# Kernel optimization log

Measured on AMD Instinct MI355X. Metric: run time of the kernel, lower is better.

The kernel has to match this reference:

```python
import jax, jax.numpy as jnp
import numpy as np

N_EMBED = 1024
HEAD_SIZE = 64
BLOCK_SIZE = 2048


def setup_inputs() -> dict:
    key = jax.random.key(0)
    kx, kk, kv = jax.random.split(key, 3)
    x = jax.random.normal(kx, (8, 2048, N_EMBED), dtype=jnp.float32)
    # nn.Linear(n_embed, head_size, bias=False): weight [head_size, n_embed]
    scale = 1.0 / np.sqrt(N_EMBED)
    W_k = jax.random.uniform(kk, (HEAD_SIZE, N_EMBED), dtype=jnp.float32, minval=-scale, maxval=scale)
    W_v = jax.random.uniform(kv, (HEAD_SIZE, N_EMBED), dtype=jnp.float32, minval=-scale, maxval=scale)
    return {"x": x, "W_k": W_k, "W_v": W_v}


def reference(x, W_k, W_v):
    # Faithful to source: q = self.key(x) (query projection is unused in the original forward)
    T = x.shape[1]
    k = jnp.einsum('btc,hc->bth', x, W_k)   # [B,T,H]
    q = k                                    # source bug: q uses key projection
    wei = jnp.einsum('bth,bsh->bts', q, k) * (HEAD_SIZE ** -0.5)  # [B,T,T]
    causal = jnp.tril(jnp.ones((T, T), dtype=bool))
    wei = jnp.where(causal, wei, -jnp.inf)
    wei = jax.nn.softmax(wei, axis=-1)
    v = jnp.einsum('btc,hc->bth', x, W_v)
    out = jnp.einsum('bts,bsh->bth', wei, v)
    return out
```

## Files before the change

kernel.cpp:

```cpp
#include <hip/hip_runtime.h>


typedef __bf16 bf16;
typedef __bf16 bf16x4 __attribute__((ext_vector_type(4)));
typedef __bf16 bf16x8 __attribute__((ext_vector_type(8)));
typedef float  floatx4 __attribute__((ext_vector_type(4)));

#define T_LEN 2048
#define HEAD  64
#define CEMB  1024

static __device__ __forceinline__ bf16x8 cvt2(float4 a, float4 b) {
    bf16x8 r;
    r[0] = (bf16)a.x; r[1] = (bf16)a.y; r[2] = (bf16)a.z; r[3] = (bf16)a.w;
    r[4] = (bf16)b.x; r[5] = (bf16)b.y; r[6] = (bf16)b.z; r[7] = (bf16)b.w;
    return r;
}

__global__ __launch_bounds__(256) void wconv_kernel(const float* __restrict__ Wk,
                                                    const float* __restrict__ Wv,
                                                    bf16* __restrict__ Wb) {
    int i = (blockIdx.x * 256 + threadIdx.x) * 4;
    const float* src = (i < 64 * 1024) ? (Wk + i) : (Wv + (i - 64 * 1024));
    float4 f = *(const float4*)src;
    bf16x4 v;
    v[0] = (bf16)f.x; v[1] = (bf16)f.y; v[2] = (bf16)f.z; v[3] = (bf16)f.w;
    *(bf16x4*)&Wb[i] = v;
}

__global__ __launch_bounds__(256) void proj_kernel(const float* __restrict__ x,
                                                   const bf16* __restrict__ Wb,
                                                   bf16* __restrict__ Kbuf,
                                                   bf16* __restrict__ Vt) {
    __shared__ __align__(16) bf16 As[2][32][72];
    __shared__ __align__(16) bf16 Bs[2][128][72];

    const int tid  = threadIdx.x;
    const int wave = tid >> 6;
    const int lane = tid & 63;
    const int quad = lane >> 4;
    const int low  = lane & 15;

    const long row0 = (long)blockIdx.x * 32;

    const int a_row = tid >> 3;
    const int a_col = (tid & 7) * 8;
    const int b_row = tid >> 1;
    const int b_col = (tid & 1) * 32;

    const float* abase = x + (row0 + a_row) * CEMB + a_col;
    const bf16*  bbase = Wb + b_row * CEMB + b_col;

    const int strip = wave & 1;
    const int nq    = (wave >> 1) * 4;

    floatx4 acc[4];
#pragma unroll
    for (int i = 0; i < 4; ++i) acc[i] = (floatx4){0.f, 0.f, 0.f, 0.f};

    float4 apf0 = ((const float4*)abase)[0], apf1 = ((const float4*)abase)[1];
    float4 bpf0 = ((const float4*)bbase)[0], bpf1 = ((const float4*)bbase)[1];
    float4 bpf2 = ((const float4*)bbase)[2], bpf3 = ((const float4*)bbase)[3];
    *(bf16x8*)&As[0][a_row][a_col] = cvt2(apf0, apf1);
    *(float4*)&Bs[0][b_row][b_col]      = bpf0;
    *(float4*)&Bs[0][b_row][b_col + 8]  = bpf1;
    *(float4*)&Bs[0][b_row][b_col + 16] = bpf2;
    *(float4*)&Bs[0][b_row][b_col + 24] = bpf3;
    __syncthreads();

    int buf = 0;
    for (int s = 0; s < 16; ++s) {
        const bool more = (s < 15);
        if (more) {
            const int k0 = (s + 1) * 64;
            apf0 = ((const float4*)(abase + k0))[0]; apf1 = ((const float4*)(abase + k0))[1];
            bpf0 = ((const float4*)(bbase + k0))[0]; bpf1 = ((const float4*)(bbase + k0))[1];
            bpf2 = ((const float4*)(bbase + k0))[2]; bpf3 = ((const float4*)(bbase + k0))[3];
        }
#pragma unroll
        for (int ks = 0; ks < 2; ++ks) {
            bf16x8 afrag = *(const bf16x8*)&As[buf][strip * 16 + low][ks * 32 + quad * 8];
#pragma unroll
            for (int i = 0; i < 4; ++i) {
                bf16x8 bfrag = *(const bf16x8*)&Bs[buf][(nq + i) * 16 + low][ks * 32 + quad * 8];
                acc[i] = __builtin_amdgcn_mfma_f32_16x16x32_bf16(afrag, bfrag, acc[i], 0, 0, 0);
            }
        }
        if (more) {
            const int nb = buf ^ 1;
            *(bf16x8*)&As[nb][a_row][a_col] = cvt2(apf0, apf1);
            *(float4*)&Bs[nb][b_row][b_col]      = bpf0;
            *(float4*)&Bs[nb][b_row][b_col + 8]  = bpf1;
            *(float4*)&Bs[nb][b_row][b_col + 16] = bpf2;
            *(float4*)&Bs[nb][b_row][b_col + 24] = bpf3;
            __syncthreads();
            buf = nb;
        }
    }

    const long bidx  = row0 >> 11;
    const int  tloc0 = (int)(row0 & 2047);
#pragma unroll
    for (int i = 0; i < 4; ++i) {
#pragma unroll
        for (int r = 0; r < 4; ++r) {
            int trow = tloc0 + strip * 16 + quad * 4 + r;
            int cl   = (nq + i) * 16 + low;
            bf16 val = (bf16)acc[i][r];
            if (cl < HEAD) Kbuf[(bidx * T_LEN + trow) * HEAD + cl] = val;
            else           Vt[(bidx * HEAD + (cl - HEAD)) * T_LEN + trow] = val;
        }
    }
}

__global__ __launch_bounds__(256) void attn_kernel(const bf16* __restrict__ Kbuf,
                                                   const bf16* __restrict__ Vt,
                                                   float* __restrict__ Opart,
                                                   float* __restrict__ lpart) {
    __shared__ __align__(16) bf16 Ks[2][64][72];
    __shared__ __align__(16) bf16 Vs[2][64][72];
    __shared__ __align__(16) bf16 Ps[64][72];

    const int tid  = threadIdx.x;
    const int wave = tid >> 6;
    const int lane = tid & 63;
    const int quad = lane >> 4;
    const int low  = lane & 15;

    const int c  = blockIdx.x & 7;
    const int qb = (blockIdx.x >> 3) & 31;
    const int b  = blockIdx.x >> 8;

    const bf16* kbase = Kbuf + (long)b * T_LEN * HEAD;
    const bf16* vbase = Vt + (long)b * HEAD * T_LEN;

    const bf16* qrow = kbase + (qb * 64 + wave * 16 + low) * HEAD + quad * 8;
    const bf16x8 qf0 = *(const bf16x8*)(qrow);
    const bf16x8 qf1 = *(const bf16x8*)(qrow + 32);

    bf16x8 ones;
#pragma unroll
    for (int i = 0; i < 8; ++i) ones[i] = (bf16)1.0f;

    floatx4 o[4], ol;
#pragma unroll
    for (int nt = 0; nt < 4; ++nt) o[nt] = (floatx4){0.f, 0.f, 0.f, 0.f};
    ol = (floatx4){0.f, 0.f, 0.f, 0.f};

    const int s_row = tid >> 2;
    const int s_col = (tid & 3) * 16;
    const bf16* ksrc = kbase + s_row * HEAD + s_col;
    const bf16* vsrc = vbase + (long)s_row * T_LEN + s_col;

    if (c <= qb) {
        float4 kpf0 = *(const float4*)(ksrc + c * 4096);
        float4 kpf1 = *(const float4*)(ksrc + c * 4096 + 8);
        float4 vpf0 = *(const float4*)(vsrc + c * 64);
        float4 vpf1 = *(const float4*)(vsrc + c * 64 + 8);
        *(float4*)&Ks[0][s_row][s_col]     = kpf0;
        *(float4*)&Ks[0][s_row][s_col + 8] = kpf1;
        *(float4*)&Vs[0][s_row][s_col]     = vpf0;
        *(float4*)&Vs[0][s_row][s_col + 8] = vpf1;
        __syncthreads();

        int buf = 0;
        for (int j = c; j <= qb; j += 8) {
            const bool more = (j + 8 <= qb);
            if (more) {
                kpf0 = *(const float4*)(ksrc + (j + 8) * 4096);
                kpf1 = *(const float4*)(ksrc + (j + 8) * 4096 + 8);
                vpf0 = *(const float4*)(vsrc + (j + 8) * 64);
                vpf1 = *(const float4*)(vsrc + (j + 8) * 64 + 8);
            }

            floatx4 s_[4];
#pragma unroll
            for (int nt = 0; nt < 4; ++nt) {
                bf16x8 kf0 = *(const bf16x8*)&Ks[buf][nt * 16 + low][quad * 8];
                bf16x8 kf1 = *(const bf16x8*)&Ks[buf][nt * 16 + low][32 + quad * 8];
                floatx4 z = (floatx4){0.f, 0.f, 0.f, 0.f};
                z = __builtin_amdgcn_mfma_f32_16x16x32_bf16(qf0, kf0, z, 0, 0, 0);
                z = __builtin_amdgcn_mfma_f32_16x16x32_bf16(qf1, kf1, z, 0, 0, 0);
                s_[nt] = z;
            }

            const bool diag = (j == qb);
#pragma unroll
            for (int nt = 0; nt < 4; ++nt) {
#pragma unroll
                for (int r = 0; r < 4; ++r) {
                    float p = __builtin_amdgcn_exp2f(s_[nt][r] * 0.180336880f);
                    if (diag && (nt * 16 + low) > (wave * 16 + quad * 4 + r)) p = 0.f;
                    Ps[wave * 16 + quad * 4 + r][nt * 16 + low] = (bf16)p;
                }
            }

            bf16x8 pf0 = *(const bf16x8*)&Ps[wave * 16 + low][quad * 8];
            bf16x8 pf1 = *(const bf16x8*)&Ps[wave * 16 + low][32 + quad * 8];
#pragma unroll
            for (int nt = 0; nt < 4; ++nt) {
                bf16x8 vf0 = *(const bf16x8*)&Vs[buf][nt * 16 + low][quad * 8];
                bf16x8 vf1 = *(const bf16x8*)&Vs[buf][nt * 16 + low][32 + quad * 8];
                o[nt] = __builtin_amdgcn_mfma_f32_16x16x32_bf16(pf0, vf0, o[nt], 0, 0, 0);
                o[nt] = __builtin_amdgcn_mfma_f32_16x16x32_bf16(pf1, vf1, o[nt], 0, 0, 0);
            }
            ol = __builtin_amdgcn_mfma_f32_16x16x32_bf16(pf0, ones, ol, 0, 0, 0);
            ol = __builtin_amdgcn_mfma_f32_16x16x32_bf16(pf1, ones, ol, 0, 0, 0);

            if (more) {
                const int nb = buf ^ 1;
                *(float4*)&Ks[nb][s_row][s_col]     = kpf0;
                *(float4*)&Ks[nb][s_row][s_col + 8] = kpf1;
                *(float4*)&Vs[nb][s_row][s_col]     = vpf0;
                *(float4*)&Vs[nb][s_row][s_col + 8] = vpf1;
                __syncthreads();
                buf = nb;
            }
        }
    }

    float* ob = Opart + (long)blockIdx.x * 4096;
#pragma unroll
    for (int nt = 0; nt < 4; ++nt) {
#pragma unroll
        for (int r = 0; r < 4; ++r) {
            int row = wave * 16 + quad * 4 + r;
            ob[row * 64 + nt * 16 + low] = o[nt][r];
        }
    }
    if (low == 0) {
#pragma unroll
        for (int r = 0; r < 4; ++r)
            lpart[(long)blockIdx.x * 64 + wave * 16 + quad * 4 + r] = ol[r];
    }
}

__global__ __launch_bounds__(256) void attn_combine(const float* __restrict__ Opart,
                                                    const float* __restrict__ lpart,
                                                    float* __restrict__ out) {
    const int tile = blockIdx.x;
    const int tid  = threadIdx.x;
    const int row  = tid >> 2;
    const int col0 = (tid & 3) * 16;

    const float* ob = Opart + (long)tile * 8 * 4096 + row * 64 + col0;
    const float* lb = lpart + (long)tile * 8 * 64 + row;

    float l = 0.f;
#pragma unroll
    for (int ch = 0; ch < 8; ++ch) l += lb[ch * 64];
    float rl = 1.0f / l;

    float4 s0 = (float4){0.f, 0.f, 0.f, 0.f}, s1 = s0, s2 = s0, s3 = s0;
#pragma unroll
    for (int ch = 0; ch < 8; ++ch) {
        const float4* p = (const float4*)(ob + ch * 4096);
        float4 a = p[0], b = p[1], c = p[2], d = p[3];
        s0.x += a.x; s0.y += a.y; s0.z += a.z; s0.w += a.w;
        s1.x += b.x; s1.y += b.y; s1.z += b.z; s1.w += b.w;
        s2.x += c.x; s2.y += c.y; s2.z += c.z; s2.w += c.w;
        s3.x += d.x; s3.y += d.y; s3.z += d.z; s3.w += d.w;
    }
    s0.x *= rl; s0.y *= rl; s0.z *= rl; s0.w *= rl;
    s1.x *= rl; s1.y *= rl; s1.z *= rl; s1.w *= rl;
    s2.x *= rl; s2.y *= rl; s2.z *= rl; s2.w *= rl;
    s3.x *= rl; s3.y *= rl; s3.z *= rl; s3.w *= rl;

    float4* op = (float4*)(out + (long)tile * 4096 + row * 64 + col0);
    op[0] = s0; op[1] = s1; op[2] = s2; op[3] = s3;
}

extern "C" void kernel_launch(void* const* d_in, const int* in_sizes, int n_in,
                              void* d_out, int out_size, void* d_ws, size_t ws_size,
                              hipStream_t stream) {
    const float* x  = (const float*)d_in[0];
    const float* Wk = (const float*)d_in[1];
    const float* Wv = (const float*)d_in[2];
    float* out = (float*)d_out;

    char* ws = (char*)d_ws;
    bf16*  Wb    = (bf16*)ws;
    bf16*  Kbuf  = (bf16*)(ws + (1 << 20));
    bf16*  Vt    = (bf16*)(ws + (3 << 20));
    float* Opart = (float*)(ws + (5 << 20));
    float* lpart = (float*)(ws + (37 << 20));

    wconv_kernel<<<128, 256, 0, stream>>>(Wk, Wv, Wb);
    proj_kernel<<<512, 256, 0, stream>>>(x, Wb, Kbuf, Vt);
    attn_kernel<<<2048, 256, 0, stream>>>(Kbuf, Vt, Opart, lpart);
    attn_combine<<<256, 256, 0, stream>>>(Opart, lpart, out);
}
```

Measured before the change: 145.2 us.

## Deepen proj prefetch, stage epilogues via LDS, halve attention split, store partials as bf16

The projection kernel now prefetches two stages ahead and writes K and V^T through shared-memory staging, so global stores are coalesced 16-byte vectors instead of scattered scalar bf16 writes. The attention kernel drops from 8 to 4 key-chunk splits per query block, halving the grid and the partial-sum traffic. Its per-wave P buffer is made private and its output is staged through LDS to write bf16 partials with vector stores. The combine kernel reads 4 bf16 partials instead of 8 fp32 ones. This cuts workspace traffic and store inefficiency, at the cost of fewer blocks for load balance across the causal triangle and lower precision in the partial outputs.

```diff
diff --git a/kernel.cpp b/kernel.cpp
--- a/kernel.cpp
+++ b/kernel.cpp
@@ -52,30 +52,45 @@
     const bf16*  bbase = Wb + b_row * CEMB + b_col;
 
     const int strip = wave & 1;
-    const int nq    = (wave >> 1) * 4;
+    const int nhalf = wave >> 1;
+    const int nq    = nhalf * 4;
 
     floatx4 acc[4];
 #pragma unroll
     for (int i = 0; i < 4; ++i) acc[i] = (floatx4){0.f, 0.f, 0.f, 0.f};
 
-    float4 apf0 = ((const float4*)abase)[0], apf1 = ((const float4*)abase)[1];
-    float4 bpf0 = ((const float4*)bbase)[0], bpf1 = ((const float4*)bbase)[1];
-    float4 bpf2 = ((const float4*)bbase)[2], bpf3 = ((const float4*)bbase)[3];
-    *(bf16x8*)&As[0][a_row][a_col] = cvt2(apf0, apf1);
-    *(float4*)&Bs[0][b_row][b_col]      = bpf0;
-    *(float4*)&Bs[0][b_row][b_col + 8]  = bpf1;
-    *(float4*)&Bs[0][b_row][b_col + 16] = bpf2;
-    *(float4*)&Bs[0][b_row][b_col + 24] = bpf3;
+    float4 apf[2][2];
+    bf16x8 bpf[2][4];
+
+    apf[0][0] = ((const float4*)abase)[0];
+    apf[0][1] = ((const float4*)abase)[1];
+#pragma unroll
+    for (int i = 0; i < 4; ++i) bpf[0][i] = *(const bf16x8*)(bbase + 8 * i);
+    *(bf16x8*)&As[0][a_row][a_col] = cvt2(apf[0][0], apf[0][1]);
+#pragma unroll
+    for (int i = 0; i < 4; ++i) *(bf16x8*)&Bs[0][b_row][b_col + 8 * i] = bpf[0][i];
+    apf[1][0] = ((const float4*)(abase + 64))[0];
+    apf[1][1] = ((const float4*)(abase + 64))[1];
+#pragma unroll
+    for (int i = 0; i < 4; ++i) bpf[1][i] = *(const bf16x8*)(bbase + 64 + 8 * i);
     __syncthreads();
 
     int buf = 0;
     for (int s = 0; s < 16; ++s) {
-        const bool more = (s < 15);
-        if (more) {
-            const int k0 = (s + 1) * 64;
-            apf0 = ((const float4*)(abase + k0))[0]; apf1 = ((const float4*)(abase + k0))[1];
-            bpf0 = ((const float4*)(bbase + k0))[0]; bpf1 = ((const float4*)(bbase + k0))[1];
-            bpf2 = ((const float4*)(bbase + k0))[2]; bpf3 = ((const float4*)(bbase + k0))[3];
+        if (s < 15) {
+            const int q  = (s + 1) & 1;
+            const int nb = buf ^ 1;
+            *(bf16x8*)&As[nb][a_row][a_col] = cvt2(apf[q][0], apf[q][1]);
+#pragma unroll
+            for (int i = 0; i < 4; ++i) *(bf16x8*)&Bs[nb][b_row][b_col + 8 * i] = bpf[q][i];
+        }
+        if (s < 14) {
+            const int q  = s & 1;
+            const int k0 = (s + 2) * 64;
+            apf[q][0] = ((const float4*)(abase + k0))[0];
+            apf[q][1] = ((const float4*)(abase + k0))[1];
+#pragma unroll
+            for (int i = 0; i < 4; ++i) bpf[q][i] = *(const bf16x8*)(bbase + k0 + 8 * i);
         }
 #pragma unroll
         for (int ks = 0; ks < 2; ++ks) {
@@ -86,40 +101,51 @@
                 acc[i] = __builtin_amdgcn_mfma_f32_16x16x32_bf16(afrag, bfrag, acc[i], 0, 0, 0);
             }
         }
-        if (more) {
-            const int nb = buf ^ 1;
-            *(bf16x8*)&As[nb][a_row][a_col] = cvt2(apf0, apf1);
-            *(float4*)&Bs[nb][b_row][b_col]      = bpf0;
-            *(float4*)&Bs[nb][b_row][b_col + 8]  = bpf1;
-            *(float4*)&Bs[nb][b_row][b_col + 16] = bpf2;
-            *(float4*)&Bs[nb][b_row][b_col + 24] = bpf3;
+        if (s < 15) {
             __syncthreads();
-            buf = nb;
-        }
-    }
+            buf ^= 1;
+        }
+    }
+
+    __syncthreads();
+    bf16* Ek = (bf16*)&Bs[0][0][0];
+    bf16* Ev = (bf16*)&Bs[1][0][0];
+    if (nhalf == 0) {
+#pragma unroll
+        for (int i = 0; i < 4; ++i)
+#pragma unroll
+            for (int r = 0; r < 4; ++r)
+                Ek[(strip * 16 + quad * 4 + r) * 72 + i * 16 + low] = (bf16)acc[i][r];
+    } else {
+#pragma unroll
+        for (int i = 0; i < 4; ++i)
+#pragma unroll
+            for (int r = 0; r < 4; ++r)
+                Ev[(i * 16 + low) * 36 + strip * 16 + quad * 4 + r] = (bf16)acc[i][r];
+    }
+    __syncthreads();
 
     const long bidx  = row0 >> 11;
     const int  tloc0 = (int)(row0 & 2047);
-#pragma unroll
-    for (int i = 0; i < 4; ++i) {
-#pragma unroll
-        for (int r = 0; r < 4; ++r) {
-            int trow = tloc0 + strip * 16 + quad * 4 + r;
-            int cl   = (nq + i) * 16 + low;
-            bf16 val = (bf16)acc[i][r];
-            if (cl < HEAD) Kbuf[(bidx * T_LEN + trow) * HEAD + cl] = val;
-            else           Vt[(bidx * HEAD + (cl - HEAD)) * T_LEN + trow] = val;
-        }
+    {
+        const int t  = tid >> 3;
+        const int h0 = (tid & 7) * 8;
+        *(bf16x8*)&Kbuf[(bidx * T_LEN + tloc0 + t) * HEAD + h0] = *(const bf16x8*)&Ek[t * 72 + h0];
+    }
+    {
+        const int h  = tid >> 2;
+        const int t0 = (tid & 3) * 8;
+        *(bf16x8*)&Vt[(bidx * HEAD + h) * T_LEN + tloc0 + t0] = *(const bf16x8*)&Ev[h * 36 + t0];
     }
 }
 
 __global__ __launch_bounds__(256) void attn_kernel(const bf16* __restrict__ Kbuf,
                                                    const bf16* __restrict__ Vt,
-                                                   float* __restrict__ Opart,
+                                                   bf16* __restrict__ Opart,
                                                    float* __restrict__ lpart) {
     __shared__ __align__(16) bf16 Ks[2][64][72];
     __shared__ __align__(16) bf16 Vs[2][64][72];
-    __shared__ __align__(16) bf16 Ps[64][72];
+    __shared__ __align__(16) bf16 Ps[4][16][72];
 
     const int tid  = threadIdx.x;
     const int wave = tid >> 6;
@@ -127,9 +153,9 @@
     const int quad = lane >> 4;
     const int low  = lane & 15;
 
-    const int c  = blockIdx.x & 7;
-    const int qb = (blockIdx.x >> 3) & 31;
-    const int b  = blockIdx.x >> 8;
+    const int c  = blockIdx.x & 3;
+    const int qb = (blockIdx.x >> 2) & 31;
+    const int b  = blockIdx.x >> 7;
 
     const bf16* kbase = Kbuf + (long)b * T_LEN * HEAD;
     const bf16* vbase = Vt + (long)b * HEAD * T_LEN;
@@ -164,13 +190,13 @@
         __syncthreads();
 
         int buf = 0;
-        for (int j = c; j <= qb; j += 8) {
-            const bool more = (j + 8 <= qb);
+        for (int j = c; j <= qb; j += 4) {
+            const bool more = (j + 4 <= qb);
             if (more) {
-                kpf0 = *(const float4*)(ksrc + (j + 8) * 4096);
-                kpf1 = *(const float4*)(ksrc + (j + 8) * 4096 + 8);
-                vpf0 = *(const float4*)(vsrc + (j + 8) * 64);
-                vpf1 = *(const float4*)(vsrc + (j + 8) * 64 + 8);
+                kpf0 = *(const float4*)(ksrc + (j + 4) * 4096);
+                kpf1 = *(const float4*)(ksrc + (j + 4) * 4096 + 8);
+                vpf0 = *(const float4*)(vsrc + (j + 4) * 64);
+                vpf1 = *(const float4*)(vsrc + (j + 4) * 64 + 8);
             }
 
             floatx4 s_[4];
@@ -191,12 +217,12 @@
                 for (int r = 0; r < 4; ++r) {
                     float p = __builtin_amdgcn_exp2f(s_[nt][r] * 0.180336880f);
                     if (diag && (nt * 16 + low) > (wave * 16 + quad * 4 + r)) p = 0.f;
-                    Ps[wave * 16 + quad * 4 + r][nt * 16 + low] = (bf16)p;
+                    Ps[wave][quad * 4 + r][nt * 16 + low] = (bf16)p;
                 }
             }
 
-            bf16x8 pf0 = *(const bf16x8*)&Ps[wave * 16 + low][quad * 8];
-            bf16x8 pf1 = *(const bf16x8*)&Ps[wave * 16 + low][32 + quad * 8];
+            bf16x8 pf0 = *(const bf16x8*)&Ps[wave][low][quad * 8];
+            bf16x8 pf1 = *(const bf16x8*)&Ps[wave][low][32 + quad * 8];
 #pragma unroll
             for (int nt = 0; nt < 4; ++nt) {
                 bf16x8 vf0 = *(const bf16x8*)&Vs[buf][nt * 16 + low][quad * 8];
@@ -219,14 +245,20 @@
         }
     }
 
-    float* ob = Opart + (long)blockIdx.x * 4096;
-#pragma unroll
-    for (int nt = 0; nt < 4; ++nt) {
-#pragma unroll
-        for (int r = 0; r < 4; ++r) {
-            int row = wave * 16 + quad * 4 + r;
-            ob[row * 64 + nt * 16 + low] = o[nt][r];
-        }
+    __syncthreads();
+    bf16* Eo = (bf16*)&Ks[0][0][0];
+#pragma unroll
+    for (int nt = 0; nt < 4; ++nt)
+#pragma unroll
+        for (int r = 0; r < 4; ++r)
+            Eo[(wave * 16 + quad * 4 + r) * 72 + nt * 16 + low] = (bf16)o[nt][r];
+    __syncthreads();
+    {
+        const int row  = tid >> 2;
+        const int col0 = (tid & 3) * 16;
+        bf16* ob = Opart + (long)blockIdx.x * 4096 + row * 64 + col0;
+        *(bf16x8*)(ob)     = *(const bf16x8*)&Eo[row * 72 + col0];
+        *(bf16x8*)(ob + 8) = *(const bf16x8*)&Eo[row * 72 + col0 + 8];
     }
     if (low == 0) {
 #pragma unroll
@@ -235,7 +267,7 @@
     }
 }
 
-__global__ __launch_bounds__(256) void attn_combine(const float* __restrict__ Opart,
+__global__ __launch_bounds__(256) void attn_combine(const bf16* __restrict__ Opart,
                                                     const float* __restrict__ lpart,
                                                     float* __restrict__ out) {
     const int tile = blockIdx.x;
@@ -243,31 +275,30 @@
     const int row  = tid >> 2;
     const int col0 = (tid & 3) * 16;
 
-    const float* ob = Opart + (long)tile * 8 * 4096 + row * 64 + col0;
-    const float* lb = lpart + (long)tile * 8 * 64 + row;
-
-    float l = 0.f;
-#pragma unroll
-    for (int ch = 0; ch < 8; ++ch) l += lb[ch * 64];
+    const bf16*  ob = Opart + (long)tile * 4 * 4096 + row * 64 + col0;
+    const float* lb = lpart + (long)tile * 4 * 64 + row;
+
+    float l = lb[0] + lb[64] + lb[128] + lb[192];
     float rl = 1.0f / l;
 
-    float4 s0 = (float4){0.f, 0.f, 0.f, 0.f}, s1 = s0, s2 = s0, s3 = s0;
-#pragma unroll
-    for (int ch = 0; ch < 8; ++ch) {
-        const float4* p = (const float4*)(ob + ch * 4096);
-        float4 a = p[0], b = p[1], c = p[2], d = p[3];
-        s0.x += a.x; s0.y += a.y; s0.z += a.z; s0.w += a.w;
-        s1.x += b.x; s1.y += b.y; s1.z += b.z; s1.w += b.w;
-        s2.x += c.x; s2.y += c.y; s2.z += c.z; s2.w += c.w;
-        s3.x += d.x; s3.y += d.y; s3.z += d.z; s3.w += d.w;
-    }
-    s0.x *= rl; s0.y *= rl; s0.z *= rl; s0.w *= rl;
-    s1.x *= rl; s1.y *= rl; s1.z *= rl; s1.w *= rl;
-    s2.x *= rl; s2.y *= rl; s2.z *= rl; s2.w *= rl;
-    s3.x *= rl; s3.y *= rl; s3.z *= rl; s3.w *= rl;
-
+    float s[16];
+#pragma unroll
+    for (int i = 0; i < 16; ++i) s[i] = 0.f;
+#pragma unroll
+    for (int ch = 0; ch < 4; ++ch) {
+        bf16x8 u0 = *(const bf16x8*)(ob + ch * 4096);
+        bf16x8 u1 = *(const bf16x8*)(ob + ch * 4096 + 8);
+#pragma unroll
+        for (int i = 0; i < 8; ++i) { s[i] += (float)u0[i]; s[8 + i] += (float)u1[i]; }
+    }
     float4* op = (float4*)(out + (long)tile * 4096 + row * 64 + col0);
-    op[0] = s0; op[1] = s1; op[2] = s2; op[3] = s3;
+#pragma unroll
+    for (int v = 0; v < 4; ++v) {
+        float4 w;
+        w.x = s[v * 4 + 0] * rl; w.y = s[v * 4 + 1] * rl;
+        w.z = s[v * 4 + 2] * rl; w.w = s[v * 4 + 3] * rl;
+        op[v] = w;
+    }
 }
 
 extern "C" void kernel_launch(void* const* d_in, const int* in_sizes, int n_in,
@@ -282,11 +313,11 @@
     bf16*  Wb    = (bf16*)ws;
     bf16*  Kbuf  = (bf16*)(ws + (1 << 20));
     bf16*  Vt    = (bf16*)(ws + (3 << 20));
-    float* Opart = (float*)(ws + (5 << 20));
-    float* lpart = (float*)(ws + (37 << 20));
+    bf16*  Opart = (bf16*)(ws + (5 << 20));
+    float* lpart = (float*)(ws + (13 << 20));
 
     wconv_kernel<<<128, 256, 0, stream>>>(Wk, Wv, Wb);
     proj_kernel<<<512, 256, 0, stream>>>(x, Wb, Kbuf, Vt);
-    attn_kernel<<<2048, 256, 0, stream>>>(Kbuf, Vt, Opart, lpart);
+    attn_kernel<<<1024, 256, 0, stream>>>(Kbuf, Vt, Opart, lpart);
     attn_combine<<<256, 256, 0, stream>>>(Opart, lpart, out);
 }
```

Result: faster. 129.4 us (-10.9%).
